# Optimization experiments

Hardware: AMD Instinct MI355X
Metric: run time of the kernel (lower is better)

The kernel has to match this reference:

```python
import jax, jax.numpy as jnp
import numpy as np

N = 4096   # num_nodes == nb_items
E = 3      # num_edge types
C = 2      # num_channels
D = 128    # basket_embed_dim
RU = 128   # rnn_units
B = 32     # batch size
L = 20     # max_seq_length
ALPHA = 0.5


def _gtconv(W, A):
    # softmax over edge types, then channel-weighted combine of adjacencies
    f = jax.nn.softmax(W, axis=1)              # [C, E]
    return jnp.einsum('ce,enm->cnm', f, A)     # [C, N, N]


def _normalize(H):
    # remove self loops, then column-degree (in-degree) inverse normalization
    eye = jnp.eye(H.shape[-1], dtype=H.dtype)
    Hn = H * (1.0 - eye)
    deg = Hn.sum(axis=1)                        # scatter_add over col -> [C, N]
    dinv = jnp.where(deg == 0, jnp.zeros_like(deg), 1.0 / deg)
    dinv = jax.lax.stop_gradient(dinv)          # original computes deg under no_grad
    return Hn * dinv[:, None, :]


def _lstm(x, h0, c0, W_ih, W_hh, b_ih, b_hh):
    # single-layer batch-first LSTM, torch gate order (i, f, g, o)
    def step(carry, xt):
        h, c = carry
        z = xt @ W_ih.T + b_ih + h @ W_hh.T + b_hh
        i, f, g, o = jnp.split(z, 4, axis=-1)
        c = jax.nn.sigmoid(f) * c + jax.nn.sigmoid(i) * jnp.tanh(g)
        h = jax.nn.sigmoid(o) * jnp.tanh(c)
        return (h, c), h
    _, ys = jax.lax.scan(step, (h0, c0), jnp.swapaxes(x, 0, 1))
    return jnp.swapaxes(ys, 0, 1)               # [B, L, RU]


def setup_inputs():
    key = jax.random.key(0)
    k = jax.random.split(key, 12)
    A = jax.random.uniform(k[0], (E, N, N), jnp.float32) * (2.0 / N)
    seqs = (jax.random.uniform(k[1], (B, L, N)) < 0.02).astype(jnp.float32)
    seq_len = jax.random.randint(k[2], (B,), 1, L + 1)
    h0 = jnp.zeros((B, RU), jnp.float32)
    c0 = jnp.zeros((B, RU), jnp.float32)
    W1a = 1.0 + 0.1 * jax.random.normal(k[3], (C, E), jnp.float32)
    W1b = 1.0 + 0.1 * jax.random.normal(k[4], (C, E), jnp.float32)
    W2 = 1.0 + 0.1 * jax.random.normal(k[5], (C, E), jnp.float32)
    I_B = jnp.ones((N,), jnp.float32) / N
    lin_w = jax.random.normal(k[6], (C, D, N), jnp.float32) / np.sqrt(N).astype(np.float32)
    lin_b = jnp.zeros((C, D), jnp.float32)
    proj_w = jax.random.normal(k[7], (D, C * D), jnp.float32) / np.sqrt(C * D).astype(np.float32)
    proj_b = jnp.zeros((D,), jnp.float32)
    W_ih = jax.random.normal(k[8], (4 * RU, D), jnp.float32) / np.sqrt(D).astype(np.float32)
    W_hh = jax.random.normal(k[9], (4 * RU, RU), jnp.float32) / np.sqrt(RU).astype(np.float32)
    b_ih = jnp.zeros((4 * RU,), jnp.float32)
    b_hh = jnp.zeros((4 * RU,), jnp.float32)
    h2item_w = jax.random.normal(k[10], (N, RU), jnp.float32) / np.sqrt(RU).astype(np.float32)
    return dict(A=A, seqs=seqs, seq_len=seq_len, h0=h0, c0=c0, W1a=W1a, W1b=W1b,
                W2=W2, I_B=I_B, lin_w=lin_w, lin_b=lin_b, proj_w=proj_w, proj_b=proj_b,
                W_ih=W_ih, W_hh=W_hh, b_ih=b_ih, b_hh=b_hh, h2item_w=h2item_w)


def reference(A, seqs, seq_len, h0, c0, W1a, W1b, W2, I_B, lin_w, lin_b,
              proj_w, proj_b, W_ih, W_hh, b_ih, b_hh, h2item_w):
    # layer 0 (first=True): H[c] = conv1(A)[c] @ conv2(A)[c]  (spspmm, dense form)
    H = jnp.einsum('cij,cjk->cik', _gtconv(W1a, A), _gtconv(W1b, A))
    # layer 1: H[c] = norm(H)[c] @ conv(A)[c]
    H = jnp.einsum('cij,cjk->cik', _normalize(H), _gtconv(W2, A))

    x = seqs.reshape(-1, N)                     # [B*L, nb_items]
    v = jax.nn.relu(I_B)                        # diag(I_B) after relu
    enc = []
    for i in range(C):
        xh = jax.nn.relu(x @ H[i])
        if i == 0:
            e = jax.nn.relu(x * v) + xh         # note: channel-0 formula differs
        else:
            e = jax.nn.relu(x * v + xh)
        enc.append(e @ lin_w[i].T + lin_b[i])
    enc = jnp.concatenate(enc, axis=1)          # [B*L, C*D]
    baskets = (enc @ proj_w.T + proj_b).reshape(B, L, D)

    lstm_out = _lstm(baskets, h0, c0, W_ih, W_hh, b_ih, b_hh)
    idx = jnp.arange(B) * L + (seq_len - 1)
    last = lstm_out.reshape(-1, RU)[idx]        # [B, RU]
    probs = jax.nn.sigmoid(last @ h2item_w.T)   # [B, nb_items]
    return (1.0 - ALPHA) * probs + ALPHA * (probs * v)
```

## Files before the change

### kernel.cpp

```cpp
#include <hip/hip_runtime.h>


typedef float  f4v  __attribute__((ext_vector_type(4)));
typedef short  s8v  __attribute__((ext_vector_type(8)));
typedef unsigned short u16;
typedef u16    us4  __attribute__((ext_vector_type(4)));

#define NN 4096
#define MM 640
#define KSPL 4
#define KCH (NN/KSPL)

__device__ __forceinline__ u16 f2bf(float f){
  unsigned int u = __float_as_uint(f);
  u += 0x7FFFu + ((u>>16)&1u);
  return (u16)(u>>16);
}
__device__ __forceinline__ float bf2f(u16 h){ return __uint_as_float(((unsigned int)h)<<16); }
__device__ __forceinline__ float sigm(float x){ return 1.f/(1.f+__expf(-x)); }

__device__ __forceinline__ void gload16(const void* g, void* l){
  __builtin_amdgcn_global_load_lds((const __attribute__((address_space(1))) unsigned int*)g,
                                   (__attribute__((address_space(3))) unsigned int*)l, 16, 0, 0);
}

__device__ __forceinline__ void softmax23(const float* __restrict__ W, float f[2][3]){
  #pragma unroll
  for (int c=0;c<2;c++){
    float a=W[c*3+0], b=W[c*3+1], d=W[c*3+2];
    float m=fmaxf(a,fmaxf(b,d));
    float ea=__expf(a-m), eb=__expf(b-m), ed=__expf(d-m);
    float s=1.f/(ea+eb+ed);
    f[c][0]=ea*s; f[c][1]=eb*s; f[c][2]=ed*s;
  }
}

__global__ __launch_bounds__(256)
void k_combine_all(const float* __restrict__ A, const float* __restrict__ W1a,
                   const float* __restrict__ W1b, const float* __restrict__ W2,
                   u16* __restrict__ C1, u16* __restrict__ C2t,
                   u16* __restrict__ C3t, float* __restrict__ r)
{
  __shared__ u16 t2[2][64][68];
  __shared__ u16 t3[2][64][68];
  __shared__ float rs[2][64];
  const int tid = threadIdx.x;
  const int n0 = blockIdx.x*64, m0 = blockIdx.y*64;
  float fa[2][3], fb[2][3], fc[2][3];
  softmax23(W1a, fa);
  softmax23(W1b, fb);
  softmax23(W2,  fc);
  if (tid < 128) rs[tid>>6][tid&63] = 0.f;
  __syncthreads();
  const int cl = (tid&15)*4, rw0 = tid>>4;
  float rp[2][4] = {};
  #pragma unroll
  for (int q=0;q<4;q++){
    const int m = q*16 + rw0;
    const float* ap = A + (size_t)(m0+m)*NN + n0 + cl;
    f4v a0 = *(const f4v*)ap;
    f4v a1 = *(const f4v*)(ap + (size_t)NN*NN);
    f4v a2 = *(const f4v*)(ap + 2*(size_t)NN*NN);
    #pragma unroll
    for (int c=0;c<2;c++){
      f4v v1 = fa[c][0]*a0 + fa[c][1]*a1 + fa[c][2]*a2;
      f4v vt = fb[c][0]*a0 + fb[c][1]*a1 + fb[c][2]*a2;
      f4v v3 = fc[c][0]*a0 + fc[c][1]*a1 + fc[c][2]*a2;
      us4 o;
      #pragma unroll
      for (int k=0;k<4;k++){ o[k]=f2bf(v1[k]); rp[c][k]+=v1[k]; }
      *(us4*)(C1 + ((size_t)c*NN + m0+m)*NN + n0+cl) = o;
      #pragma unroll
      for (int k=0;k<4;k++){ t2[c][cl+k][m] = f2bf(vt[k]); t3[c][cl+k][m] = f2bf(v3[k]); }
    }
  }
  #pragma unroll
  for (int c=0;c<2;c++)
    #pragma unroll
    for (int k=0;k<4;k++) atomicAdd(&rs[c][cl+k], rp[c][k]);
  __syncthreads();
  if (tid < 128) atomicAdd(&r[(size_t)(tid>>6)*NN + n0 + (tid&63)], rs[tid>>6][tid&63]);
  #pragma unroll
  for (int q=0;q<4;q++){
    const int nl = q*16 + rw0;
    #pragma unroll
    for (int c=0;c<2;c++){
      us4 o2 = *(const us4*)&t2[c][nl][cl];
      us4 o3 = *(const us4*)&t3[c][nl][cl];
      *(us4*)(C2t + ((size_t)c*NN + n0+nl)*NN + m0+cl) = o2;
      *(us4*)(C3t + ((size_t)c*NN + n0+nl)*NN + m0+cl) = o3;
    }
  }
}

__global__ __launch_bounds__(256)
void k_sparse_y(const float* __restrict__ seqs, const u16* __restrict__ C1,
                u16* __restrict__ y)
{
  __shared__ int idxl[512];
  __shared__ int cnt;
  const int tid = threadIdx.x, row = blockIdx.x;
  if (tid==0) cnt = 0;
  __syncthreads();
  const float* xr = seqs + (size_t)row*NN;
  #pragma unroll
  for (int it=0; it<4; ++it){
    f4v v = *(const f4v*)(xr + it*1024 + tid*4);
    #pragma unroll
    for (int k=0;k<4;k++) if (v[k] > 0.5f){ int p = atomicAdd(&cnt,1); if (p<512) idxl[p] = it*1024+tid*4+k; }
  }
  __syncthreads();
  const int nz = cnt < 512 ? cnt : 512;
  float acc0[16], acc1[16];
  #pragma unroll
  for (int k=0;k<16;k++){ acc0[k]=0.f; acc1[k]=0.f; }
  const int cb = tid*16;
  for (int p=0;p<nz;++p){
    const u16* r0 = C1 + (size_t)idxl[p]*NN + cb;
    const u16* r1 = r0 + (size_t)NN*NN;
    s8v a = *(const s8v*)r0, b = *(const s8v*)(r0+8);
    s8v c = *(const s8v*)r1, d = *(const s8v*)(r1+8);
    #pragma unroll
    for (int k=0;k<8;k++){
      acc0[k]   += bf2f((u16)a[k]);
      acc0[8+k] += bf2f((u16)b[k]);
      acc1[k]   += bf2f((u16)c[k]);
      acc1[8+k] += bf2f((u16)d[k]);
    }
  }
  s8v o0,o1,o2,o3;
  #pragma unroll
  for (int k=0;k<8;k++){
    o0[k]=(short)f2bf(acc0[k]);   o1[k]=(short)f2bf(acc0[8+k]);
    o2[k]=(short)f2bf(acc1[k]);   o3[k]=(short)f2bf(acc1[8+k]);
  }
  u16* y0 = y + (size_t)row*NN + cb;
  *(s8v*)y0 = o0; *(s8v*)(y0+8) = o1;
  u16* y1 = y0 + (size_t)MM*NN;
  *(s8v*)y1 = o2; *(s8v*)(y1+8) = o3;
}

__global__ __launch_bounds__(256)
void k_diagdeg(const u16* __restrict__ C1, const u16* __restrict__ C2t,
               const float* __restrict__ r, float* __restrict__ diag1,
               float* __restrict__ dinv)
{
  const int tid = threadIdx.x, lane = tid&63;
  const int gw = blockIdx.x*4 + (tid>>6);
  const int c = gw>>12, k = gw&4095;
  const u16* p1 = C1  + ((size_t)c*NN + k)*NN;
  const u16* p2 = C2t + ((size_t)c*NN + k)*NN;
  const float* pr = r + (size_t)c*NN;
  float dd = 0.f, dg = 0.f;
  for (int it=0; it<8; ++it){
    const int j = it*512 + lane*8;
    s8v v1 = *(const s8v*)(p1+j);
    s8v v2 = *(const s8v*)(p2+j);
    f4v r0 = *(const f4v*)(pr+j);
    f4v r1 = *(const f4v*)(pr+j+4);
    #pragma unroll
    for (int q=0;q<8;q++){
      float c2 = bf2f((u16)v2[q]);
      dd += bf2f((u16)v1[q]) * c2;
      dg += ((q<4)? r0[q] : r1[q-4]) * c2;
    }
  }
  #pragma unroll
  for (int m=1;m<64;m<<=1){ dd += __shfl_xor(dd, m); dg += __shfl_xor(dg, m); }
  if (lane==0){
    float deg = dg - dd;
    diag1[(size_t)c*NN+k] = dd;
    dinv[(size_t)c*NN+k]  = (deg==0.f) ? 0.f : 1.f/deg;
  }
}

__global__ __launch_bounds__(256)
void k_gemm_sk(const u16* __restrict__ Xb, const u16* __restrict__ Bt,
               float* __restrict__ part)
{
  __shared__ u16 As[128*64];
  __shared__ u16 Bs[128*64];
  const int tid = threadIdx.x, lane = tid&63, w = tid>>6;
  const int m0 = blockIdx.x*128, n0 = blockIdx.y*128;
  const int c = blockIdx.z>>2, ks = blockIdx.z&3;
  const u16* Ab = Xb + (size_t)c*MM*NN;
  const u16* Bb = Bt + (size_t)c*NN*NN;
  const int srow = lane>>3;
  const int scol = ((lane&7) ^ srow)*8;
  const int fr = lane&15, fkq = lane>>4;
  const int wm = (w>>1)*64, wn = (w&1)*64;
  f4v acc[4][4] = {};
  const int kbase = ks*KCH;
  for (int k0=0;k0<KCH;k0+=64){
    #pragma unroll
    for (int t=0;t<4;t++){
      gload16(Ab + (size_t)(m0 + t*32 + w*8 + srow)*NN + kbase + k0 + scol, (void*)&As[(t*32 + w*8)*64]);
      gload16(Bb + (size_t)(n0 + t*32 + w*8 + srow)*NN + kbase + k0 + scol, (void*)&Bs[(t*32 + w*8)*64]);
    }
    __syncthreads();
    #pragma unroll
    for (int kk=0;kk<2;kk++){
      s8v a[4], b[4];
      #pragma unroll
      for (int t=0;t<4;t++){
        const int ra = wm + t*16 + fr;
        a[t] = *(const s8v*)&As[ra*64 + (((kk*4 + fkq) ^ (ra&7))*8)];
        const int rb = wn + t*16 + fr;
        b[t] = *(const s8v*)&Bs[rb*64 + (((kk*4 + fkq) ^ (rb&7))*8)];
      }
      #pragma unroll
      for (int i=0;i<4;i++)
        #pragma unroll
        for (int j=0;j<4;j++)
          acc[i][j] = __builtin_amdgcn_mfma_f32_16x16x32_bf16(a[i], b[j], acc[i][j], 0, 0, 0);
    }
    __syncthreads();
  }
  float* pb = part + (size_t)blockIdx.z*MM*NN;
  #pragma unroll
  for (int i=0;i<4;i++){
    #pragma unroll
    for (int j=0;j<4;j++){
      const int col = n0 + wn + j*16 + fr;
      #pragma unroll
      for (int rr=0;rr<4;rr++){
        const int row = m0 + wm + i*16 + (lane>>4)*4 + rr;
        pb[(size_t)row*NN + col] = acc[i][j][rr];
      }
    }
  }
}

template<int EPI>
__global__ __launch_bounds__(256)
void k_epi(const float* __restrict__ part, const float* __restrict__ seqs,
           const float* __restrict__ diag1, const float* __restrict__ dinv,
           const float* __restrict__ IB, u16* __restrict__ outp)
{
  const int g = blockIdx.x*256 + threadIdx.x;
  const int c = blockIdx.y;
  const int row = g>>10, colq = g&1023;
  const int col = colq*4;
  const size_t base = (size_t)row*NN + col;
  f4v z = {0.f,0.f,0.f,0.f};
  #pragma unroll
  for (int ks=0;ks<KSPL;ks++)
    z += *(const f4v*)(part + (size_t)(c*KSPL+ks)*MM*NN + base);
  f4v x = *(const f4v*)(seqs + base);
  f4v val;
  if constexpr(EPI==0){
    f4v d  = *(const f4v*)(diag1 + (size_t)c*NN + col);
    f4v dv = *(const f4v*)(dinv  + (size_t)c*NN + col);
    val = (z - x*d) * dv;
  } else {
    f4v ib = *(const f4v*)(IB + col);
    #pragma unroll
    for (int k=0;k<4;k++){
      float xh = fmaxf(z[k], 0.f);
      float vv = fmaxf(ib[k], 0.f);
      val[k] = (c==0) ? (fmaxf(x[k]*vv,0.f) + xh) : fmaxf(x[k]*vv + xh, 0.f);
    }
  }
  us4 o;
  #pragma unroll
  for (int k=0;k<4;k++) o[k]=f2bf(val[k]);
  *(us4*)(outp + (size_t)c*MM*NN + base) = o;
}

__global__ __launch_bounds__(256)
void k_cvt(const float* __restrict__ linw, const float* __restrict__ whh,
           u16* __restrict__ linwb, u16* __restrict__ whhb)
{
  const int g = blockIdx.x*256 + threadIdx.x;
  const int i = g*4;
  const int NL = 2*128*NN;
  f4v v; u16* dst;
  if (i < NL){ v = *(const f4v*)(linw + i); dst = linwb + i; }
  else       { v = *(const f4v*)(whh + (i-NL)); dst = whhb + (i-NL); }
  us4 o;
  #pragma unroll
  for (int k=0;k<4;k++) o[k]=f2bf(v[k]);
  *(us4*)dst = o;
}

__global__ __launch_bounds__(256)
void k_lin(const u16* __restrict__ e, const u16* __restrict__ linwb,
           float* __restrict__ encr)
{
  __shared__ u16 As[64*32];
  __shared__ u16 Bs[64*32];
  const int tid=threadIdx.x, lane=tid&63, w=tid>>6;
  const int m0 = blockIdx.x*64, d0 = blockIdx.y*64;
  const int c = blockIdx.z>>2, ks = blockIdx.z&3;
  const u16* Ab = e + (size_t)c*MM*NN;
  const u16* Bb = linwb + (size_t)c*128*NN;
  const int srow=lane>>2, skof=(lane&3)*8, fr=lane&15, fk=(lane>>4)*8;
  const int wm=(w>>1)*32, wn=(w&1)*32;
  f4v acc[2][2];
  #pragma unroll
  for (int i=0;i<2;i++)
    #pragma unroll
    for (int j=0;j<2;j++) acc[i][j] = (f4v){0.f,0.f,0.f,0.f};
  for (int ki=0;ki<32;++ki){
    const int k0 = ks*1024 + ki*32;
    gload16(Ab + (size_t)(m0 + w*16 + srow)*NN + k0 + skof, (void*)&As[(w*16)*32]);
    gload16(Bb + (size_t)(d0 + w*16 + srow)*NN + k0 + skof, (void*)&Bs[(w*16)*32]);
    __syncthreads();
    s8v a[2], b[2];
    #pragma unroll
    for (int t=0;t<2;t++) a[t] = *(const s8v*)&As[(wm+t*16+fr)*32+fk];
    #pragma unroll
    for (int t=0;t<2;t++) b[t] = *(const s8v*)&Bs[(wn+t*16+fr)*32+fk];
    #pragma unroll
    for (int i=0;i<2;i++)
      #pragma unroll
      for (int j=0;j<2;j++)
        acc[i][j] = __builtin_amdgcn_mfma_f32_16x16x32_bf16(a[i], b[j], acc[i][j], 0, 0, 0);
    __syncthreads();
  }
  #pragma unroll
  for (int i=0;i<2;i++)
    #pragma unroll
    for (int j=0;j<2;j++){
      const int col = d0 + wn + j*16 + fr;
      #pragma unroll
      for (int rr=0;rr<4;rr++){
        const int row = m0 + wm + i*16 + (lane>>4)*4 + rr;
        atomicAdd(&encr[(size_t)row*256 + c*128 + col], acc[i][j][rr]);
      }
    }
}

__global__ __launch_bounds__(256)
void k_proj(const float* __restrict__ encr, const float* __restrict__ linb,
            const float* __restrict__ pw, const float* __restrict__ pb,
            float* __restrict__ bask)
{
  const int g = blockIdx.x*256 + threadIdx.x;
  const int row = g>>7, d = g&127;
  const float* er = encr + (size_t)row*256;
  const float* wr = pw + (size_t)d*256;
  float acc = pb[d];
  for (int j=0;j<256;j+=4){
    f4v e4 = *(const f4v*)(er+j);
    f4v l4 = *(const f4v*)(linb+j);
    f4v w4 = *(const f4v*)(wr+j);
    acc += (e4[0]+l4[0])*w4[0] + (e4[1]+l4[1])*w4[1] + (e4[2]+l4[2])*w4[2] + (e4[3]+l4[3])*w4[3];
  }
  bask[g] = acc;
}

__global__ __launch_bounds__(256)
void k_xhat(const float* __restrict__ bask, const float* __restrict__ wih,
            const float* __restrict__ bih, const float* __restrict__ bhh,
            float* __restrict__ xh)
{
  const int g = blockIdx.x*256 + threadIdx.x;
  const int row = g>>9, n = g&511;
  const float* br = bask + (size_t)row*128;
  const float* wr = wih + (size_t)n*128;
  float acc = bih[n] + bhh[n];
  for (int k=0;k<128;k+=4){
    f4v b4=*(const f4v*)(br+k); f4v w4=*(const f4v*)(wr+k);
    acc += b4[0]*w4[0]+b4[1]*w4[1]+b4[2]*w4[2]+b4[3]*w4[3];
  }
  const int b = row/20, t = row%20;
  xh[((size_t)t*32 + b)*512 + n] = acc;
}

__global__ __launch_bounds__(512)
void k_lstm(const float* __restrict__ xhat, const u16* __restrict__ whhb,
            const float* __restrict__ h0, const float* __restrict__ c0,
            const int* __restrict__ slen, float* __restrict__ last)
{
  __shared__ float zb[32][512];
  __shared__ float cbuf[32][128];
  __shared__ u16 hb[32][136];
  const int tid = threadIdx.x, lane = tid&63, w = tid>>6;
  for (int i=tid; i<4096; i+=512){ int b=i>>7,u=i&127; cbuf[b][u]=c0[i]; hb[b][u]=f2bf(h0[i]); }
  const int fr = lane&15, fko = (lane>>4)*8;
  s8v bfr[4][4];
  #pragma unroll
  for (int nt=0;nt<4;nt++)
    #pragma unroll
    for (int kf=0;kf<4;kf++)
      bfr[nt][kf] = *(const s8v*)(whhb + (size_t)(w*64 + nt*16 + fr)*128 + kf*32 + fko);
  __syncthreads();
  for (int t=0;t<20;++t){
    s8v af[2][4];
    #pragma unroll
    for (int mt=0;mt<2;mt++)
      #pragma unroll
      for (int kf=0;kf<4;kf++)
        af[mt][kf] = *(const s8v*)&hb[mt*16+fr][kf*32+fko];
    f4v z[2][4];
    #pragma unroll
    for (int mt=0;mt<2;mt++)
      #pragma unroll
      for (int nt=0;nt<4;nt++){
        const int nn2 = w*64 + nt*16 + fr;
        #pragma unroll
        for (int rr=0;rr<4;rr++){
          const int bb = mt*16 + (lane>>4)*4 + rr;
          z[mt][nt][rr] = xhat[((size_t)t*32 + bb)*512 + nn2];
        }
      }
    #pragma unroll
    for (int kf=0;kf<4;kf++)
      #pragma unroll
      for (int mt=0;mt<2;mt++)
        #pragma unroll
        for (int nt=0;nt<4;nt++)
          z[mt][nt] = __builtin_amdgcn_mfma_f32_16x16x32_bf16(af[mt][kf], bfr[nt][kf], z[mt][nt], 0, 0, 0);
    #pragma unroll
    for (int mt=0;mt<2;mt++)
      #pragma unroll
      for (int nt=0;nt<4;nt++){
        const int nn2 = w*64 + nt*16 + fr;
        #pragma unroll
        for (int rr=0;rr<4;rr++){
          const int bb = mt*16 + (lane>>4)*4 + rr;
          zb[bb][nn2] = z[mt][nt][rr];
        }
      }
    __syncthreads();
    for (int p=tid; p<4096; p+=512){
      const int b=p>>7, u=p&127;
      float zi=zb[b][u], zf=zb[b][128+u], zg=zb[b][256+u], zo=zb[b][384+u];
      float ii=sigm(zi), ff=sigm(zf), gg=tanhf(zg), oo=sigm(zo);
      float cn = ff*cbuf[b][u] + ii*gg;
      float hn = oo*tanhf(cn);
      cbuf[b][u]=cn; hb[b][u]=f2bf(hn);
      if (t == slen[b]-1) last[p] = hn;
    }
    __syncthreads();
  }
}

__global__ __launch_bounds__(256)
void k_final(const float* __restrict__ last, const float* __restrict__ h2w,
             const float* __restrict__ IB, float* __restrict__ out)
{
  __shared__ float ls[128];
  const int b = blockIdx.y;
  const int n = blockIdx.x*256 + threadIdx.x;
  if (threadIdx.x < 128) ls[threadIdx.x] = last[b*128 + threadIdx.x];
  __syncthreads();
  const float* wr = h2w + (size_t)n*128;
  float acc = 0.f;
  for (int k=0;k<128;k+=4){
    f4v w4 = *(const f4v*)(wr+k);
    acc += w4[0]*ls[k] + w4[1]*ls[k+1] + w4[2]*ls[k+2] + w4[3]*ls[k+3];
  }
  const float vn = fmaxf(IB[n], 0.f);
  out[(size_t)b*NN + n] = (0.5f + 0.5f*vn) * sigm(acc);
}

extern "C" void kernel_launch(void* const* d_in, const int* in_sizes, int n_in,
                              void* d_out, int out_size, void* d_ws, size_t ws_size,
                              hipStream_t stream)
{
  const float* A    = (const float*)d_in[0];
  const float* seqs = (const float*)d_in[1];
  const int*   slen = (const int*)  d_in[2];
  const float* h0   = (const float*)d_in[3];
  const float* c0   = (const float*)d_in[4];
  const float* W1a  = (const float*)d_in[5];
  const float* W1b  = (const float*)d_in[6];
  const float* W2   = (const float*)d_in[7];
  const float* IB   = (const float*)d_in[8];
  const float* linw = (const float*)d_in[9];
  const float* linb = (const float*)d_in[10];
  const float* pw   = (const float*)d_in[11];
  const float* pb   = (const float*)d_in[12];
  const float* wih  = (const float*)d_in[13];
  const float* whh  = (const float*)d_in[14];
  const float* bih  = (const float*)d_in[15];
  const float* bhh  = (const float*)d_in[16];
  const float* h2w  = (const float*)d_in[17];
  (void)in_sizes; (void)n_in; (void)out_size; (void)ws_size;

  char* ws = (char*)d_ws;
  size_t off = 0;
  auto alloc = [&](size_t sz)->void*{ void* p = ws + off; off += (sz + 255) & ~(size_t)255; return p; };
  u16*   C1    = (u16*)  alloc((size_t)2*NN*NN*2);
  u16*   C2t   = (u16*)  alloc((size_t)2*NN*NN*2);
  u16*   C3t   = (u16*)  alloc((size_t)2*NN*NN*2);
  u16*   y     = (u16*)  alloc((size_t)2*MM*NN*2);
  u16*   u     = (u16*)  alloc((size_t)2*MM*NN*2);
  float* part  = (float*)alloc((size_t)2*KSPL*MM*NN*4);
  float* r     = (float*)alloc((size_t)2*NN*4);
  float* diag1 = (float*)alloc((size_t)2*NN*4);
  float* dinv  = (float*)alloc((size_t)2*NN*4);
  u16*   linwb = (u16*)  alloc((size_t)2*128*NN*2);
  u16*   whhb  = (u16*)  alloc((size_t)512*128*2);
  float* encr  = (float*)alloc((size_t)MM*256*4);
  float* bask  = (float*)alloc((size_t)MM*128*4);
  float* xh    = (float*)alloc((size_t)20*32*512*4);
  float* last  = (float*)alloc((size_t)32*128*4);

  hipMemsetAsync(r, 0, (size_t)2*NN*4, stream);
  hipMemsetAsync(encr, 0, (size_t)MM*256*4, stream);

  k_combine_all<<<dim3(64,64),256,0,stream>>>(A, W1a, W1b, W2, C1, C2t, C3t, r);
  k_sparse_y<<<MM,256,0,stream>>>(seqs, C1, y);
  k_diagdeg<<<2048,256,0,stream>>>(C1, C2t, r, diag1, dinv);
  k_gemm_sk<<<dim3(5,32,2*KSPL),256,0,stream>>>(y, C2t, part);
  k_epi<0><<<dim3(2560,2),256,0,stream>>>(part, seqs, diag1, dinv, IB, u);
  k_gemm_sk<<<dim3(5,32,2*KSPL),256,0,stream>>>(u, C3t, part);
  u16* e = y;
  k_epi<1><<<dim3(2560,2),256,0,stream>>>(part, seqs, diag1, dinv, IB, e);
  k_cvt<<<1088,256,0,stream>>>(linw, whh, linwb, whhb);
  k_lin<<<dim3(10,2,8),256,0,stream>>>(e, linwb, encr);
  k_proj<<<320,256,0,stream>>>(encr, linb, pw, pb, bask);
  k_xhat<<<1280,256,0,stream>>>(bask, wih, bih, bhh, xh);
  k_lstm<<<1,512,0,stream>>>(xh, whhb, h0, c0, slen, last);
  k_final<<<dim3(16,32),256,0,stream>>>(last, h2w, IB, (float*)d_out);
}
```

Baseline: 575.9 us.

## Replace sparse gather with dense GEMM, retile split-K GEMM with XCD-aware mapping

Drops the sparse row-gather kernel. The first product seqs @ C1 is now a dense bf16 MFMA GEMM against a newly written transposed C1 copy (C1t), with seqs converted to bf16 in a small kernel. The split-K GEMM moves from 4-way to 2-way split and from 64-wide to 32-wide K tiles, and uses a 1D grid whose block index maps column tiles by XCD for L2 locality. Also uses the packed v_cvt_pk_bf16_f32 instruction for bf16 conversion, restructures the combine kernel's transposes, and deepens the k_lin split-K. The cost is an extra 64MB C1t write and a full dense GEMM in place of a sparse sum over about 2% nonzeros.

```diff
diff --git a/kernel.cpp b/kernel.cpp
--- a/kernel.cpp
+++ b/kernel.cpp
@@ -4,12 +4,12 @@
 typedef float  f4v  __attribute__((ext_vector_type(4)));
 typedef short  s8v  __attribute__((ext_vector_type(8)));
 typedef unsigned short u16;
-typedef u16    us4  __attribute__((ext_vector_type(4)));
+typedef unsigned int u32;
+typedef u32    u2v  __attribute__((ext_vector_type(2)));
+typedef u32    u4v  __attribute__((ext_vector_type(4)));
 
 #define NN 4096
 #define MM 640
-#define KSPL 4
-#define KCH (NN/KSPL)
 
 __device__ __forceinline__ u16 f2bf(float f){
   unsigned int u = __float_as_uint(f);
@@ -18,6 +18,12 @@
 }
 __device__ __forceinline__ float bf2f(u16 h){ return __uint_as_float(((unsigned int)h)<<16); }
 __device__ __forceinline__ float sigm(float x){ return 1.f/(1.f+__expf(-x)); }
+
+__device__ __forceinline__ u32 pkbf(float lo, float hi){
+  u32 r;
+  asm("v_cvt_pk_bf16_f32 %0, %1, %2" : "=v"(r) : "v"(lo), "v"(hi));
+  return r;
+}
 
 __device__ __forceinline__ void gload16(const void* g, void* l){
   __builtin_amdgcn_global_load_lds((const __attribute__((address_space(1))) unsigned int*)g,
@@ -38,106 +44,80 @@
 __global__ __launch_bounds__(256)
 void k_combine_all(const float* __restrict__ A, const float* __restrict__ W1a,
                    const float* __restrict__ W1b, const float* __restrict__ W2,
-                   u16* __restrict__ C1, u16* __restrict__ C2t,
-                   u16* __restrict__ C3t, float* __restrict__ r)
-{
-  __shared__ u16 t2[2][64][68];
-  __shared__ u16 t3[2][64][68];
+                   u16* __restrict__ C1, u16* __restrict__ C1t,
+                   u16* __restrict__ C2t, u16* __restrict__ C3t,
+                   float* __restrict__ r)
+{
+  __shared__ u16 t1[64][72];
+  __shared__ u16 t2[64][72];
+  __shared__ u16 t3[64][72];
   __shared__ float rs[2][64];
-  const int tid = threadIdx.x;
+  const int tid = threadIdx.x, lane = tid&63;
   const int n0 = blockIdx.x*64, m0 = blockIdx.y*64;
   float fa[2][3], fb[2][3], fc[2][3];
-  softmax23(W1a, fa);
-  softmax23(W1b, fb);
-  softmax23(W2,  fc);
+  softmax23(W1a, fa); softmax23(W1b, fb); softmax23(W2, fc);
   if (tid < 128) rs[tid>>6][tid&63] = 0.f;
-  __syncthreads();
-  const int cl = (tid&15)*4, rw0 = tid>>4;
-  float rp[2][4] = {};
-  #pragma unroll
-  for (int q=0;q<4;q++){
-    const int m = q*16 + rw0;
-    const float* ap = A + (size_t)(m0+m)*NN + n0 + cl;
-    f4v a0 = *(const f4v*)ap;
-    f4v a1 = *(const f4v*)(ap + (size_t)NN*NN);
-    f4v a2 = *(const f4v*)(ap + 2*(size_t)NN*NN);
-    #pragma unroll
-    for (int c=0;c<2;c++){
-      f4v v1 = fa[c][0]*a0 + fa[c][1]*a1 + fa[c][2]*a2;
-      f4v vt = fb[c][0]*a0 + fb[c][1]*a1 + fb[c][2]*a2;
-      f4v v3 = fc[c][0]*a0 + fc[c][1]*a1 + fc[c][2]*a2;
-      us4 o;
-      #pragma unroll
-      for (int k=0;k<4;k++){ o[k]=f2bf(v1[k]); rp[c][k]+=v1[k]; }
-      *(us4*)(C1 + ((size_t)c*NN + m0+m)*NN + n0+cl) = o;
-      #pragma unroll
-      for (int k=0;k<4;k++){ t2[c][cl+k][m] = f2bf(vt[k]); t3[c][cl+k][m] = f2bf(v3[k]); }
-    }
-  }
-  #pragma unroll
-  for (int c=0;c<2;c++)
-    #pragma unroll
-    for (int k=0;k<4;k++) atomicAdd(&rs[c][cl+k], rp[c][k]);
-  __syncthreads();
+  const int mb = tid>>4, nb = tid&15;
+  f4v a0[4], a1[4], a2[4];
+  #pragma unroll
+  for (int j=0;j<4;j++){
+    const float* ap = A + (size_t)(m0+mb*4+j)*NN + n0 + nb*4;
+    a0[j] = *(const f4v*)ap;
+    a1[j] = *(const f4v*)(ap + (size_t)NN*NN);
+    a2[j] = *(const f4v*)(ap + 2*(size_t)NN*NN);
+  }
+  #pragma unroll
+  for (int c=0;c<2;c++){
+    float rp[4] = {};
+    #pragma unroll
+    for (int j=0;j<4;j++){
+      f4v v1 = fa[c][0]*a0[j] + fa[c][1]*a1[j] + fa[c][2]*a2[j];
+      u2v o = { pkbf(v1[0],v1[1]), pkbf(v1[2],v1[3]) };
+      *(u2v*)(C1 + ((size_t)c*NN + m0+mb*4+j)*NN + n0 + nb*4) = o;
+      #pragma unroll
+      for (int k=0;k<4;k++) rp[k] += v1[k];
+    }
+    #pragma unroll
+    for (int jj=0;jj<4;jj++){
+      f4v c1v, c2v, c3v;
+      #pragma unroll
+      for (int j=0;j<4;j++){
+        c1v[j] = fa[c][0]*a0[j][jj] + fa[c][1]*a1[j][jj] + fa[c][2]*a2[j][jj];
+        c2v[j] = fb[c][0]*a0[j][jj] + fb[c][1]*a1[j][jj] + fb[c][2]*a2[j][jj];
+        c3v[j] = fc[c][0]*a0[j][jj] + fc[c][1]*a1[j][jj] + fc[c][2]*a2[j][jj];
+      }
+      *(u2v*)&t1[nb*4+jj][mb*4] = (u2v){ pkbf(c1v[0],c1v[1]), pkbf(c1v[2],c1v[3]) };
+      *(u2v*)&t2[nb*4+jj][mb*4] = (u2v){ pkbf(c2v[0],c2v[1]), pkbf(c2v[2],c2v[3]) };
+      *(u2v*)&t3[nb*4+jj][mb*4] = (u2v){ pkbf(c3v[0],c3v[1]), pkbf(c3v[2],c3v[3]) };
+    }
+    __syncthreads();
+    #pragma unroll
+    for (int rep=0;rep<2;rep++){
+      const int rw = rep*32 + (tid>>3), l8 = tid&7;
+      *(u4v*)(C1t + ((size_t)c*NN + n0+rw)*NN + m0 + l8*8) = *(const u4v*)&t1[rw][l8*8];
+      *(u4v*)(C2t + ((size_t)c*NN + n0+rw)*NN + m0 + l8*8) = *(const u4v*)&t2[rw][l8*8];
+      *(u4v*)(C3t + ((size_t)c*NN + n0+rw)*NN + m0 + l8*8) = *(const u4v*)&t3[rw][l8*8];
+    }
+    #pragma unroll
+    for (int k=0;k<4;k++){
+      float v = rp[k];
+      v += __shfl_xor(v,16); v += __shfl_xor(v,32);
+      if (lane < 16) atomicAdd(&rs[c][nb*4+k], v);
+    }
+    __syncthreads();
+  }
   if (tid < 128) atomicAdd(&r[(size_t)(tid>>6)*NN + n0 + (tid&63)], rs[tid>>6][tid&63]);
-  #pragma unroll
-  for (int q=0;q<4;q++){
-    const int nl = q*16 + rw0;
-    #pragma unroll
-    for (int c=0;c<2;c++){
-      us4 o2 = *(const us4*)&t2[c][nl][cl];
-      us4 o3 = *(const us4*)&t3[c][nl][cl];
-      *(us4*)(C2t + ((size_t)c*NN + n0+nl)*NN + m0+cl) = o2;
-      *(us4*)(C3t + ((size_t)c*NN + n0+nl)*NN + m0+cl) = o3;
-    }
-  }
-}
-
-__global__ __launch_bounds__(256)
-void k_sparse_y(const float* __restrict__ seqs, const u16* __restrict__ C1,
-                u16* __restrict__ y)
-{
-  __shared__ int idxl[512];
-  __shared__ int cnt;
-  const int tid = threadIdx.x, row = blockIdx.x;
-  if (tid==0) cnt = 0;
-  __syncthreads();
-  const float* xr = seqs + (size_t)row*NN;
-  #pragma unroll
-  for (int it=0; it<4; ++it){
-    f4v v = *(const f4v*)(xr + it*1024 + tid*4);
-    #pragma unroll
-    for (int k=0;k<4;k++) if (v[k] > 0.5f){ int p = atomicAdd(&cnt,1); if (p<512) idxl[p] = it*1024+tid*4+k; }
-  }
-  __syncthreads();
-  const int nz = cnt < 512 ? cnt : 512;
-  float acc0[16], acc1[16];
-  #pragma unroll
-  for (int k=0;k<16;k++){ acc0[k]=0.f; acc1[k]=0.f; }
-  const int cb = tid*16;
-  for (int p=0;p<nz;++p){
-    const u16* r0 = C1 + (size_t)idxl[p]*NN + cb;
-    const u16* r1 = r0 + (size_t)NN*NN;
-    s8v a = *(const s8v*)r0, b = *(const s8v*)(r0+8);
-    s8v c = *(const s8v*)r1, d = *(const s8v*)(r1+8);
-    #pragma unroll
-    for (int k=0;k<8;k++){
-      acc0[k]   += bf2f((u16)a[k]);
-      acc0[8+k] += bf2f((u16)b[k]);
-      acc1[k]   += bf2f((u16)c[k]);
-      acc1[8+k] += bf2f((u16)d[k]);
-    }
-  }
-  s8v o0,o1,o2,o3;
-  #pragma unroll
-  for (int k=0;k<8;k++){
-    o0[k]=(short)f2bf(acc0[k]);   o1[k]=(short)f2bf(acc0[8+k]);
-    o2[k]=(short)f2bf(acc1[k]);   o3[k]=(short)f2bf(acc1[8+k]);
-  }
-  u16* y0 = y + (size_t)row*NN + cb;
-  *(s8v*)y0 = o0; *(s8v*)(y0+8) = o1;
-  u16* y1 = y0 + (size_t)MM*NN;
-  *(s8v*)y1 = o2; *(s8v*)(y1+8) = o3;
+}
+
+__global__ __launch_bounds__(256)
+void k_cvtx(const float* __restrict__ seqs, u16* __restrict__ xb)
+{
+  const int g = blockIdx.x*256 + threadIdx.x;
+  const int i = g*4;
+  f4v v = *(const f4v*)(seqs + i);
+  u2v o = { pkbf(v[0],v[1]), pkbf(v[2],v[3]) };
+  *(u2v*)(xb + i) = o;
+  *(u2v*)(xb + (size_t)MM*NN + i) = o;
 }
 
 __global__ __launch_bounds__(256)
@@ -178,45 +158,46 @@
 void k_gemm_sk(const u16* __restrict__ Xb, const u16* __restrict__ Bt,
                float* __restrict__ part)
 {
-  __shared__ u16 As[128*64];
-  __shared__ u16 Bs[128*64];
+  __shared__ u16 As[128*32];
+  __shared__ u16 Bs[128*32];
   const int tid = threadIdx.x, lane = tid&63, w = tid>>6;
-  const int m0 = blockIdx.x*128, n0 = blockIdx.y*128;
-  const int c = blockIdx.z>>2, ks = blockIdx.z&3;
+  const int g = blockIdx.x;
+  const int xcd = g & 7, q = g >> 3;
+  const int m = q % 5, p = q / 5;
+  const int nn = p & 3, ks = (p>>2)&1, c = p>>3;
+  const int m0 = m*128, n0 = (nn*8 + xcd)*128, kb = ks*2048;
   const u16* Ab = Xb + (size_t)c*MM*NN;
   const u16* Bb = Bt + (size_t)c*NN*NN;
-  const int srow = lane>>3;
-  const int scol = ((lane&7) ^ srow)*8;
-  const int fr = lane&15, fkq = lane>>4;
+  const int srow = lane>>2;
+  const int scol = ((lane&3) ^ ((lane>>3)&3))*8;
+  const int fr = lane&15, c0 = lane>>4;
+  const int key = (fr>>1)&3;
   const int wm = (w>>1)*64, wn = (w&1)*64;
   f4v acc[4][4] = {};
-  const int kbase = ks*KCH;
-  for (int k0=0;k0<KCH;k0+=64){
+  for (int k0=0;k0<2048;k0+=32){
+    #pragma unroll
+    for (int i=0;i<2;i++){
+      const int rbase = i*64 + w*16;
+      gload16(Ab + (size_t)(m0 + rbase + srow)*NN + kb + k0 + scol, (void*)&As[rbase*32]);
+      gload16(Bb + (size_t)(n0 + rbase + srow)*NN + kb + k0 + scol, (void*)&Bs[rbase*32]);
+    }
+    __syncthreads();
+    s8v a[4], b[4];
     #pragma unroll
     for (int t=0;t<4;t++){
-      gload16(Ab + (size_t)(m0 + t*32 + w*8 + srow)*NN + kbase + k0 + scol, (void*)&As[(t*32 + w*8)*64]);
-      gload16(Bb + (size_t)(n0 + t*32 + w*8 + srow)*NN + kbase + k0 + scol, (void*)&Bs[(t*32 + w*8)*64]);
-    }
-    __syncthreads();
-    #pragma unroll
-    for (int kk=0;kk<2;kk++){
-      s8v a[4], b[4];
-      #pragma unroll
-      for (int t=0;t<4;t++){
-        const int ra = wm + t*16 + fr;
-        a[t] = *(const s8v*)&As[ra*64 + (((kk*4 + fkq) ^ (ra&7))*8)];
-        const int rb = wn + t*16 + fr;
-        b[t] = *(const s8v*)&Bs[rb*64 + (((kk*4 + fkq) ^ (rb&7))*8)];
-      }
-      #pragma unroll
-      for (int i=0;i<4;i++)
-        #pragma unroll
-        for (int j=0;j<4;j++)
-          acc[i][j] = __builtin_amdgcn_mfma_f32_16x16x32_bf16(a[i], b[j], acc[i][j], 0, 0, 0);
-    }
-    __syncthreads();
-  }
-  float* pb = part + (size_t)blockIdx.z*MM*NN;
+      const int ra = wm + t*16 + fr;
+      a[t] = *(const s8v*)&As[ra*32 + ((c0 ^ key)*8)];
+      const int rb = wn + t*16 + fr;
+      b[t] = *(const s8v*)&Bs[rb*32 + ((c0 ^ key)*8)];
+    }
+    #pragma unroll
+    for (int i=0;i<4;i++)
+      #pragma unroll
+      for (int j=0;j<4;j++)
+        acc[i][j] = __builtin_amdgcn_mfma_f32_16x16x32_bf16(a[i], b[j], acc[i][j], 0, 0, 0);
+    __syncthreads();
+  }
+  float* pb = part + (size_t)(c*2+ks)*MM*NN;
   #pragma unroll
   for (int i=0;i<4;i++){
     #pragma unroll
@@ -231,7 +212,7 @@
   }
 }
 
-template<int EPI>
+template<int M>
 __global__ __launch_bounds__(256)
 void k_epi(const float* __restrict__ part, const float* __restrict__ seqs,
            const float* __restrict__ diag1, const float* __restrict__ dinv,
@@ -239,20 +220,20 @@
 {
   const int g = blockIdx.x*256 + threadIdx.x;
   const int c = blockIdx.y;
-  const int row = g>>10, colq = g&1023;
-  const int col = colq*4;
+  const int row = g>>10, col = (g&1023)*4;
   const size_t base = (size_t)row*NN + col;
-  f4v z = {0.f,0.f,0.f,0.f};
-  #pragma unroll
-  for (int ks=0;ks<KSPL;ks++)
-    z += *(const f4v*)(part + (size_t)(c*KSPL+ks)*MM*NN + base);
-  f4v x = *(const f4v*)(seqs + base);
+  f4v z = *(const f4v*)(part + (size_t)(c*2+0)*MM*NN + base)
+        + *(const f4v*)(part + (size_t)(c*2+1)*MM*NN + base);
   f4v val;
-  if constexpr(EPI==0){
+  if constexpr(M==0){
+    val = z;
+  } else if constexpr(M==1){
+    f4v x  = *(const f4v*)(seqs + base);
     f4v d  = *(const f4v*)(diag1 + (size_t)c*NN + col);
     f4v dv = *(const f4v*)(dinv  + (size_t)c*NN + col);
     val = (z - x*d) * dv;
   } else {
+    f4v x  = *(const f4v*)(seqs + base);
     f4v ib = *(const f4v*)(IB + col);
     #pragma unroll
     for (int k=0;k<4;k++){
@@ -261,10 +242,8 @@
       val[k] = (c==0) ? (fmaxf(x[k]*vv,0.f) + xh) : fmaxf(x[k]*vv + xh, 0.f);
     }
   }
-  us4 o;
-  #pragma unroll
-  for (int k=0;k<4;k++) o[k]=f2bf(val[k]);
-  *(us4*)(outp + (size_t)c*MM*NN + base) = o;
+  u2v o = { pkbf(val[0],val[1]), pkbf(val[2],val[3]) };
+  *(u2v*)(outp + (size_t)c*MM*NN + base) = o;
 }
 
 __global__ __launch_bounds__(256)
@@ -277,10 +256,8 @@
   f4v v; u16* dst;
   if (i < NL){ v = *(const f4v*)(linw + i); dst = linwb + i; }
   else       { v = *(const f4v*)(whh + (i-NL)); dst = whhb + (i-NL); }
-  us4 o;
-  #pragma unroll
-  for (int k=0;k<4;k++) o[k]=f2bf(v[k]);
-  *(us4*)dst = o;
+  u2v o = { pkbf(v[0],v[1]), pkbf(v[2],v[3]) };
+  *(u2v*)dst = o;
 }
 
 __global__ __launch_bounds__(256)
@@ -291,7 +268,7 @@
   __shared__ u16 Bs[64*32];
   const int tid=threadIdx.x, lane=tid&63, w=tid>>6;
   const int m0 = blockIdx.x*64, d0 = blockIdx.y*64;
-  const int c = blockIdx.z>>2, ks = blockIdx.z&3;
+  const int c = blockIdx.z>>4, ks = blockIdx.z&15;
   const u16* Ab = e + (size_t)c*MM*NN;
   const u16* Bb = linwb + (size_t)c*128*NN;
   const int srow=lane>>2, skof=(lane&3)*8, fr=lane&15, fk=(lane>>4)*8;
@@ -301,8 +278,8 @@
   for (int i=0;i<2;i++)
     #pragma unroll
     for (int j=0;j<2;j++) acc[i][j] = (f4v){0.f,0.f,0.f,0.f};
-  for (int ki=0;ki<32;++ki){
-    const int k0 = ks*1024 + ki*32;
+  for (int ki=0;ki<8;++ki){
+    const int k0 = ks*256 + ki*32;
     gload16(Ab + (size_t)(m0 + w*16 + srow)*NN + k0 + skof, (void*)&As[(w*16)*32]);
     gload16(Bb + (size_t)(d0 + w*16 + srow)*NN + k0 + skof, (void*)&Bs[(w*16)*32]);
     __syncthreads();
@@ -484,11 +461,14 @@
   size_t off = 0;
   auto alloc = [&](size_t sz)->void*{ void* p = ws + off; off += (sz + 255) & ~(size_t)255; return p; };
   u16*   C1    = (u16*)  alloc((size_t)2*NN*NN*2);
+  u16*   C1t   = (u16*)  alloc((size_t)2*NN*NN*2);
   u16*   C2t   = (u16*)  alloc((size_t)2*NN*NN*2);
   u16*   C3t   = (u16*)  alloc((size_t)2*NN*NN*2);
+  u16*   xb    = (u16*)  alloc((size_t)2*MM*NN*2);
   u16*   y     = (u16*)  alloc((size_t)2*MM*NN*2);
   u16*   u     = (u16*)  alloc((size_t)2*MM*NN*2);
-  float* part  = (float*)alloc((size_t)2*KSPL*MM*NN*4);
+  u16*   e     = (u16*)  alloc((size_t)2*MM*NN*2);
+  float* part  = (float*)alloc((size_t)2*2*MM*NN*4);
   float* r     = (float*)alloc((size_t)2*NN*4);
   float* diag1 = (float*)alloc((size_t)2*NN*4);
   float* dinv  = (float*)alloc((size_t)2*NN*4);
@@ -502,16 +482,17 @@
   hipMemsetAsync(r, 0, (size_t)2*NN*4, stream);
   hipMemsetAsync(encr, 0, (size_t)MM*256*4, stream);
 
-  k_combine_all<<<dim3(64,64),256,0,stream>>>(A, W1a, W1b, W2, C1, C2t, C3t, r);
-  k_sparse_y<<<MM,256,0,stream>>>(seqs, C1, y);
+  k_combine_all<<<dim3(64,64),256,0,stream>>>(A, W1a, W1b, W2, C1, C1t, C2t, C3t, r);
+  k_cvtx<<<2560,256,0,stream>>>(seqs, xb);
   k_diagdeg<<<2048,256,0,stream>>>(C1, C2t, r, diag1, dinv);
-  k_gemm_sk<<<dim3(5,32,2*KSPL),256,0,stream>>>(y, C2t, part);
-  k_epi<0><<<dim3(2560,2),256,0,stream>>>(part, seqs, diag1, dinv, IB, u);
-  k_gemm_sk<<<dim3(5,32,2*KSPL),256,0,stream>>>(u, C3t, part);
-  u16* e = y;
-  k_epi<1><<<dim3(2560,2),256,0,stream>>>(part, seqs, diag1, dinv, IB, e);
+  k_gemm_sk<<<640,256,0,stream>>>(xb, C1t, part);
+  k_epi<0><<<dim3(2560,2),256,0,stream>>>(part, seqs, diag1, dinv, IB, y);
+  k_gemm_sk<<<640,256,0,stream>>>(y, C2t, part);
+  k_epi<1><<<dim3(2560,2),256,0,stream>>>(part, seqs, diag1, dinv, IB, u);
+  k_gemm_sk<<<640,256,0,stream>>>(u, C3t, part);
+  k_epi<2><<<dim3(2560,2),256,0,stream>>>(part, seqs, diag1, dinv, IB, e);
   k_cvt<<<1088,256,0,stream>>>(linw, whh, linwb, whhb);
-  k_lin<<<dim3(10,2,8),256,0,stream>>>(e, linwb, encr);
+  k_lin<<<dim3(10,2,32),256,0,stream>>>(e, linwb, encr);
   k_proj<<<320,256,0,stream>>>(encr, linb, pw, pb, bask);
   k_xhat<<<1280,256,0,stream>>>(bask, wih, bih, bhh, xh);
   k_lstm<<<1,512,0,stream>>>(xh, whhb, h0, c0, slen, last);
```

New measurement: 624.0 us. 1.08x slower.
